# Performance work log

Measured on AMD Instinct MI355X. Metric: run time of the kernel, lower is better.

Reference implementation:

```python
import jax, jax.numpy as jnp
import numpy as np

DIM = 512
K = 64          # num_clusters
GHOST = 1
ALPHA = 100.0
EPS = 1e-12


def _l2norm(v, axis):
    return v / jnp.maximum(jnp.linalg.norm(v, axis=axis, keepdims=True), EPS)


def setup_inputs() -> dict:
    key = jax.random.key(0)
    k_x, k_c = jax.random.split(key)
    x = jax.random.normal(k_x, (64, DIM, 32, 32), dtype=jnp.float32)
    # centroids ~ orthogonal init in torch; random normal rows, unit-ish scale
    centroids = jax.random.normal(k_c, (K + GHOST, DIM), dtype=jnp.float32) / np.sqrt(DIM)
    conv_w = 2.0 * ALPHA * centroids            # [K+g, C] (1x1 conv kernel squeezed)
    conv_b = -ALPHA * jnp.linalg.norm(centroids, axis=1)  # [K+g]
    return {"x": x, "centroids": centroids, "conv_w": conv_w, "conv_b": conv_b}


def reference(x, centroids, conv_w, conv_b):
    N, C, H, W = x.shape
    L = H * W
    # descriptor-wise L2 normalization over channel dim
    xn = _l2norm(x, axis=1)
    xf = xn.reshape(N, C, L)                                   # [N, C, L]
    # 1x1 conv == per-location matmul; softmax over clusters
    logits = jnp.einsum('kc,ncl->nkl', conv_w, xf) + conv_b[None, :, None]
    a = jax.nn.softmax(logits, axis=1)                         # [N, K+g, L]
    # vlad[n,k,c] = sum_l a[n,k,l]*(x[n,c,l]-cent[k,c])
    #            = (a @ x^T) - (sum_l a) * cent   -- avoids NxKxCxL tensor
    weighted = jnp.einsum('nkl,ncl->nkc', a, xf)               # [N, K+g, C]
    a_sum = jnp.sum(a, axis=-1)                                # [N, K+g]
    vlad = weighted - a_sum[:, :, None] * centroids[None]      # [N, K+g, C]
    vlad = vlad[:, :K, :]                                      # drop ghost clusters
    vlad = _l2norm(vlad, axis=2)                               # intra-normalization
    vlad = vlad.reshape(N, K * C)
    vlad = _l2norm(vlad, axis=1)                               # global L2
    return vlad
```

## Files before the change

### kernel.cpp

```cpp
#include <hip/hip_runtime.h>
#include <hip/hip_bf16.h>

#define C_DIM 512
#define L_DIM 1024
#define KK 64
#define KG 65
#define KP 80

using f32x4  = __attribute__((ext_vector_type(4))) float;
using bf16x8 = __attribute__((ext_vector_type(8))) short;

union U4 { uint4 u; bf16x8 b; };

__device__ __forceinline__ unsigned bfh(float x) { return __float_as_uint(x) >> 16; }
__device__ __forceinline__ float bfh_f(float x) { return __uint_as_float(__float_as_uint(x) & 0xFFFF0000u); }

__device__ __forceinline__ unsigned pack2(float a, float b) {
    return __builtin_amdgcn_perm(__float_as_uint(b), __float_as_uint(a), 0x07060302u);
}

__global__ void k_prep(const float* __restrict__ conv_w, const float* __restrict__ conv_b,
                       unsigned short* __restrict__ wpH, unsigned short* __restrict__ wpL,
                       float* __restrict__ wb)
{
    int ch = blockIdx.x;
    int kt = blockIdx.y;
    int t  = threadIdx.x;
    for (int p = 0; p < 2; ++p) {
        int idx = p * 256 + t;
        int lane = idx >> 3, j = idx & 7;
        int k = kt * 16 + (lane & 15);
        int c = ch * 32 + (lane >> 4) * 8 + j;
        float v = (k < KG) ? conv_w[k * C_DIM + c] : 0.f;
        unsigned h = bfh(v);
        float r = v - __uint_as_float(h << 16);
        int pos = ((ch * 5 + kt) << 9) + idx;
        wpH[pos] = (unsigned short)h;
        wpL[pos] = (unsigned short)bfh(r);
    }
    if (ch == 0 && kt == 0 && t < KP) wb[t] = (t < KG) ? conv_b[t] : -1e30f;
}

__global__ __launch_bounds__(256) void k_s1(
    const float* __restrict__ x, const unsigned short* __restrict__ wpH,
    const unsigned short* __restrict__ wpL, const float* __restrict__ wb,
    unsigned short* __restrict__ aPh, unsigned short* __restrict__ aPl,
    float* __restrict__ asum_part)
{
    const int lb = blockIdx.x, n = blockIdx.y;
    const int t = threadIdx.x, lane = t & 63, w = t >> 6;
    const int arow = lane & 15;
    const int agrp = lane >> 4;
    const int lw0 = lb * 128 + w * 32;

    const float* xbase = x + (size_t)n * C_DIM * L_DIM;

    f32x4 acc[5][2];
#pragma unroll
    for (int a = 0; a < 5; ++a)
#pragma unroll
        for (int b = 0; b < 2; ++b) acc[a][b] = (f32x4)0.f;
    float ss0 = 0.f, ss1 = 0.f;

    for (int ch = 0; ch < 16; ++ch) {
        const int c0 = ch * 32;
        float e0[8], e1[8];
#pragma unroll
        for (int j = 0; j < 8; ++j) {
            const float* col = &xbase[(size_t)(c0 + agrp * 8 + j) * L_DIM + lw0 + arow];
            e0[j] = col[0];
            e1[j] = col[16];
        }
#pragma unroll
        for (int j = 0; j < 8; ++j) { ss0 += e0[j] * e0[j]; ss1 += e1[j] * e1[j]; }
        U4 bh[2], bl[2];
        bh[0].u.x = pack2(e0[0], e0[1]); bh[0].u.y = pack2(e0[2], e0[3]);
        bh[0].u.z = pack2(e0[4], e0[5]); bh[0].u.w = pack2(e0[6], e0[7]);
        bh[1].u.x = pack2(e1[0], e1[1]); bh[1].u.y = pack2(e1[2], e1[3]);
        bh[1].u.z = pack2(e1[4], e1[5]); bh[1].u.w = pack2(e1[6], e1[7]);
        float r0, r1, r2, r3;
        r0 = e0[0] - bfh_f(e0[0]); r1 = e0[1] - bfh_f(e0[1]);
        r2 = e0[2] - bfh_f(e0[2]); r3 = e0[3] - bfh_f(e0[3]);
        bl[0].u.x = pack2(r0, r1); bl[0].u.y = pack2(r2, r3);
        r0 = e0[4] - bfh_f(e0[4]); r1 = e0[5] - bfh_f(e0[5]);
        r2 = e0[6] - bfh_f(e0[6]); r3 = e0[7] - bfh_f(e0[7]);
        bl[0].u.z = pack2(r0, r1); bl[0].u.w = pack2(r2, r3);
        r0 = e1[0] - bfh_f(e1[0]); r1 = e1[1] - bfh_f(e1[1]);
        r2 = e1[2] - bfh_f(e1[2]); r3 = e1[3] - bfh_f(e1[3]);
        bl[1].u.x = pack2(r0, r1); bl[1].u.y = pack2(r2, r3);
        r0 = e1[4] - bfh_f(e1[4]); r1 = e1[5] - bfh_f(e1[5]);
        r2 = e1[6] - bfh_f(e1[6]); r3 = e1[7] - bfh_f(e1[7]);
        bl[1].u.z = pack2(r0, r1); bl[1].u.w = pack2(r2, r3);
        U4 ah[5], al[5];
#pragma unroll
        for (int kt = 0; kt < 5; ++kt) {
            int poff = (((ch * 5 + kt) << 6) + lane) << 3;
            ah[kt].u = *reinterpret_cast<const uint4*>(&wpH[poff]);
            al[kt].u = *reinterpret_cast<const uint4*>(&wpL[poff]);
        }
#pragma unroll
        for (int kt = 0; kt < 5; ++kt)
#pragma unroll
            for (int lt = 0; lt < 2; ++lt) {
                acc[kt][lt] = __builtin_amdgcn_mfma_f32_16x16x32_bf16(ah[kt].b, bh[lt].b, acc[kt][lt], 0, 0, 0);
                acc[kt][lt] = __builtin_amdgcn_mfma_f32_16x16x32_bf16(ah[kt].b, bl[lt].b, acc[kt][lt], 0, 0, 0);
                acc[kt][lt] = __builtin_amdgcn_mfma_f32_16x16x32_bf16(al[kt].b, bh[lt].b, acc[kt][lt], 0, 0, 0);
            }
    }

    ss0 += __shfl_xor(ss0, 16, 64); ss0 += __shfl_xor(ss0, 32, 64);
    ss1 += __shfl_xor(ss1, 16, 64); ss1 += __shfl_xor(ss1, 32, 64);
    float invc[2];
    invc[0] = 1.0f / fmaxf(sqrtf(ss0), 1e-12f);
    invc[1] = 1.0f / fmaxf(sqrtf(ss1), 1e-12f);

    float4 wbv[5];
#pragma unroll
    for (int kt = 0; kt < 5; ++kt)
        wbv[kt] = *reinterpret_cast<const float4*>(&wb[kt * 16 + agrp * 4]);

    float aval[5][2][4];
    float rs[2];
#pragma unroll
    for (int lt = 0; lt < 2; ++lt) {
        float m = -1e30f;
#pragma unroll
        for (int kt = 0; kt < 5; ++kt)
#pragma unroll
            for (int r = 0; r < 4; ++r) {
                float lg = acc[kt][lt][r] * invc[lt] + ((const float*)&wbv[kt])[r];
                aval[kt][lt][r] = lg;
                m = fmaxf(m, lg);
            }
        m = fmaxf(m, __shfl_xor(m, 16, 64));
        m = fmaxf(m, __shfl_xor(m, 32, 64));
        float s = 0.f;
#pragma unroll
        for (int kt = 0; kt < 5; ++kt)
#pragma unroll
            for (int r = 0; r < 4; ++r) {
                float e = __expf(aval[kt][lt][r] - m);
                aval[kt][lt][r] = e;
                s += e;
            }
        s += __shfl_xor(s, 16, 64);
        s += __shfl_xor(s, 32, 64);
        rs[lt] = 1.0f / s;
    }

#pragma unroll
    for (int kt = 0; kt < 4; ++kt)
#pragma unroll
        for (int r = 0; r < 4; ++r) {
            int k = kt * 16 + agrp * 4 + r;
            float s01 = 0.f;
#pragma unroll
            for (int lt = 0; lt < 2; ++lt) {
                float a = aval[kt][lt][r] * rs[lt];
                aval[kt][lt][r] = a;
                s01 += a;
            }
#pragma unroll
            for (int off = 8; off; off >>= 1) s01 += __shfl_xor(s01, off, 64);
            if ((lane & 15) == 0)
                asum_part[((n * 8 + lb) * 4 + w) * KK + k] = s01;
#pragma unroll
            for (int lt = 0; lt < 2; ++lt) {
                float ap = aval[kt][lt][r] * invc[lt];
                unsigned h = bfh(ap);
                float res = ap - __uint_as_float(h << 16);
                int idx = (n * KK + k) * L_DIM + lw0 + lt * 16 + arow;
                aPh[idx] = (unsigned short)h;
                aPl[idx] = (unsigned short)bfh(res);
            }
        }
}

#define S2P 72
__global__ __launch_bounds__(256) void k_s2(
    const float* __restrict__ x, const unsigned short* __restrict__ aPh,
    const unsigned short* __restrict__ aPl, float* __restrict__ weighted)
{
    __shared__ unsigned short Ah[64 * S2P], Al[64 * S2P];
    __shared__ unsigned short Bh[64 * S2P], Bl[64 * S2P];

    const int flat = blockIdx.x;
    const int cq = flat >> 6;
    const int n  = ((flat & 7) << 3) | ((flat >> 3) & 7);
    const int t = threadIdx.x, lane = t & 63, w = t >> 6;
    const int arow = lane & 15, agrp = lane >> 4;

    f32x4 acc[4];
#pragma unroll
    for (int a = 0; a < 4; ++a) acc[a] = (f32x4)0.f;

    for (int step = 0; step < 16; ++step) {
        const int l0 = step * 64;
        __syncthreads();
#pragma unroll
        for (int p = 0; p < 2; ++p) {
            int idx = p * 256 + t;
            int k = idx >> 3;
            int lc = (idx & 7) * 8;
            size_t g = (size_t)(n * KK + k) * L_DIM + l0 + lc;
            *reinterpret_cast<uint4*>(&Ah[k * S2P + lc]) = *reinterpret_cast<const uint4*>(&aPh[g]);
            *reinterpret_cast<uint4*>(&Al[k * S2P + lc]) = *reinterpret_cast<const uint4*>(&aPl[g]);
        }
#pragma unroll
        for (int p = 0; p < 4; ++p) {
            int idx = p * 256 + t;
            int c = idx >> 4;
            int lc = (idx & 15) * 4;
            float4 v = *reinterpret_cast<const float4*>(
                &x[((size_t)n * C_DIM + cq * 64 + c) * L_DIM + l0 + lc]);
            uint2 hw, lw;
            hw.x = pack2(v.x, v.y); hw.y = pack2(v.z, v.w);
            float r0 = v.x - bfh_f(v.x), r1 = v.y - bfh_f(v.y);
            float r2 = v.z - bfh_f(v.z), r3 = v.w - bfh_f(v.w);
            lw.x = pack2(r0, r1); lw.y = pack2(r2, r3);
            *reinterpret_cast<uint2*>(&Bh[c * S2P + lc]) = hw;
            *reinterpret_cast<uint2*>(&Bl[c * S2P + lc]) = lw;
        }
        __syncthreads();
#pragma unroll
        for (int ks = 0; ks < 2; ++ks) {
            const int koff = ks * 32 + agrp * 8;
            U4 bh, bl;
            bh.u = *reinterpret_cast<const uint4*>(&Bh[(w * 16 + arow) * S2P + koff]);
            bl.u = *reinterpret_cast<const uint4*>(&Bl[(w * 16 + arow) * S2P + koff]);
#pragma unroll
            for (int kt = 0; kt < 4; ++kt) {
                U4 ah, al;
                ah.u = *reinterpret_cast<const uint4*>(&Ah[(kt * 16 + arow) * S2P + koff]);
                al.u = *reinterpret_cast<const uint4*>(&Al[(kt * 16 + arow) * S2P + koff]);
                acc[kt] = __builtin_amdgcn_mfma_f32_16x16x32_bf16(ah.b, bh.b, acc[kt], 0, 0, 0);
                acc[kt] = __builtin_amdgcn_mfma_f32_16x16x32_bf16(ah.b, bl.b, acc[kt], 0, 0, 0);
                acc[kt] = __builtin_amdgcn_mfma_f32_16x16x32_bf16(al.b, bh.b, acc[kt], 0, 0, 0);
            }
        }
    }
#pragma unroll
    for (int kt = 0; kt < 4; ++kt)
#pragma unroll
        for (int r = 0; r < 4; ++r) {
            int k = kt * 16 + agrp * 4 + r;
            weighted[((size_t)n * KK + k) * C_DIM + cq * 64 + w * 16 + arow] = acc[kt][r];
        }
}

__global__ void k_rownorm(const float* __restrict__ weighted, const float* __restrict__ part,
                          const float* __restrict__ cent, float* __restrict__ a_sum,
                          float* __restrict__ rn)
{
    int nk = blockIdx.x;
    int n = nk >> 6, k = nk & 63;
    int t = threadIdx.x;
    float as = 0.f;
#pragma unroll
    for (int p = 0; p < 32; ++p) as += part[(n * 32 + p) * KK + k];
    if (t == 0) a_sum[nk] = as;
    float s = 0.f;
    for (int c = t; c < C_DIM; c += 256) {
        float v = weighted[(size_t)nk * C_DIM + c] - as * cent[k * C_DIM + c];
        s += v * v;
    }
#pragma unroll
    for (int off = 32; off; off >>= 1) s += __shfl_down(s, off, 64);
    __shared__ float red[4];
    if ((t & 63) == 0) red[t >> 6] = s;
    __syncthreads();
    if (t == 0) rn[nk] = red[0] + red[1] + red[2] + red[3];
}

__global__ void k_scale(const float* __restrict__ rn, float* __restrict__ scale)
{
    int n = blockIdx.x;
    int k = threadIdx.x;
    float s = rn[n * 64 + k];
    float nrm = sqrtf(s);
    float den = fmaxf(nrm, 1e-12f);
    float tk = nrm / den;
    float tot = tk * tk;
#pragma unroll
    for (int off = 32; off; off >>= 1) tot += __shfl_down(tot, off, 64);
    tot = __shfl(tot, 0, 64);
    float g = fmaxf(sqrtf(tot), 1e-12f);
    scale[n * 64 + k] = 1.0f / (den * g);
}

__global__ void k_out(const float* __restrict__ weighted, const float* __restrict__ a_sum,
                      const float* __restrict__ cent, const float* __restrict__ scale,
                      float* __restrict__ out)
{
    int nk = blockIdx.x;
    int k = nk & 63;
    int t = threadIdx.x;
    float as = a_sum[nk];
    float sc = scale[nk];
    for (int c = t; c < C_DIM; c += 256) {
        float v = weighted[(size_t)nk * C_DIM + c] - as * cent[k * C_DIM + c];
        out[(size_t)nk * C_DIM + c] = v * sc;
    }
}

extern "C" void kernel_launch(void* const* d_in, const int* in_sizes, int n_in,
                              void* d_out, int out_size, void* d_ws, size_t ws_size,
                              hipStream_t stream)
{
    const float* x    = (const float*)d_in[0];
    const float* cent = (const float*)d_in[1];
    const float* cw   = (const float*)d_in[2];
    const float* cb   = (const float*)d_in[3];
    float* out = (float*)d_out;
    char* ws = (char*)d_ws;

    unsigned short* wpH = (unsigned short*)(ws + 0);
    unsigned short* wpL = (unsigned short*)(ws + 131072);
    float*          wb  = (float*)(ws + 262144);
    unsigned short* aPh = (unsigned short*)(ws + 524288);
    unsigned short* aPl = (unsigned short*)(ws + 8912896);
    float* asum_part    = (float*)(ws + 17301504);
    float* a_sum        = (float*)(ws + 17825792);
    float* weighted     = (float*)(ws + 18874368);
    float* rn           = (float*)(ws + 35651584);
    float* scale        = (float*)(ws + 35667968);

    k_prep<<<dim3(16, 5), 256, 0, stream>>>(cw, cb, wpH, wpL, wb);
    k_s1<<<dim3(8, 64), 256, 0, stream>>>(x, wpH, wpL, wb, aPh, aPl, asum_part);
    k_s2<<<512, 256, 0, stream>>>(x, aPh, aPl, weighted);
    k_rownorm<<<4096, 256, 0, stream>>>(weighted, asum_part, cent, a_sum, rn);
    k_scale<<<64, 64, 0, stream>>>(rn, scale);
    k_out<<<4096, 256, 0, stream>>>(weighted, a_sum, cent, scale, out);
}
```

Baseline: 78.45 us.

## Split first-stage logits GEMM over channel halves with partial-sum reduction kernel

The logits stage is split into two kernels. The first runs twice as many blocks, each covering half the channel range, and writes partial MFMA accumulators and squared-norm sums to workspace. The second kernel adds the two partials and then does the softmax and packing. This is meant to fill the GPU better than 512 blocks did, at the cost of an extra launch and an extra round trip of partials through global memory.

```diff
diff --git a/kernel.cpp b/kernel.cpp
--- a/kernel.cpp
+++ b/kernel.cpp
@@ -18,6 +18,8 @@
 __device__ __forceinline__ unsigned pack2(float a, float b) {
     return __builtin_amdgcn_perm(__float_as_uint(b), __float_as_uint(a), 0x07060302u);
 }
+
+#define PB 2688
 
 __global__ void k_prep(const float* __restrict__ conv_w, const float* __restrict__ conv_b,
                        unsigned short* __restrict__ wpH, unsigned short* __restrict__ wpL,
@@ -41,13 +43,12 @@
     if (ch == 0 && kt == 0 && t < KP) wb[t] = (t < KG) ? conv_b[t] : -1e30f;
 }
 
-__global__ __launch_bounds__(256) void k_s1(
+__global__ __launch_bounds__(256) void k_s1a(
     const float* __restrict__ x, const unsigned short* __restrict__ wpH,
-    const unsigned short* __restrict__ wpL, const float* __restrict__ wb,
-    unsigned short* __restrict__ aPh, unsigned short* __restrict__ aPl,
-    float* __restrict__ asum_part)
-{
-    const int lb = blockIdx.x, n = blockIdx.y;
+    const unsigned short* __restrict__ wpL, float* __restrict__ pacc)
+{
+    const int bx = blockIdx.x, n = blockIdx.y;
+    const int lb = bx >> 1, chalf = bx & 1;
     const int t = threadIdx.x, lane = t & 63, w = t >> 6;
     const int arow = lane & 15;
     const int agrp = lane >> 4;
@@ -62,7 +63,8 @@
         for (int b = 0; b < 2; ++b) acc[a][b] = (f32x4)0.f;
     float ss0 = 0.f, ss1 = 0.f;
 
-    for (int ch = 0; ch < 16; ++ch) {
+    for (int ch8 = 0; ch8 < 8; ++ch8) {
+        const int ch = chalf * 8 + ch8;
         const int c0 = ch * 32;
         float e0[8], e1[8];
 #pragma unroll
@@ -108,6 +110,48 @@
             }
     }
 
+    float* p = pacc + ((size_t)(n * 16 + bx) * 4 + w) * PB;
+#pragma unroll
+    for (int kt = 0; kt < 5; ++kt)
+#pragma unroll
+        for (int lt = 0; lt < 2; ++lt)
+            *reinterpret_cast<float4*>(&p[(kt * 2 + lt) * 256 + lane * 4]) =
+                make_float4(acc[kt][lt][0], acc[kt][lt][1], acc[kt][lt][2], acc[kt][lt][3]);
+    *reinterpret_cast<float2*>(&p[2560 + lane * 2]) = make_float2(ss0, ss1);
+}
+
+__global__ __launch_bounds__(256) void k_s1b(
+    const float* __restrict__ pacc, const float* __restrict__ wb,
+    unsigned short* __restrict__ aPh, unsigned short* __restrict__ aPl,
+    float* __restrict__ asum_part)
+{
+    const int lb = blockIdx.x, n = blockIdx.y;
+    const int t = threadIdx.x, lane = t & 63, w = t >> 6;
+    const int arow = lane & 15;
+    const int agrp = lane >> 4;
+    const int lw0 = lb * 128 + w * 32;
+
+    f32x4 acc[5][2];
+    float ss0 = 0.f, ss1 = 0.f;
+#pragma unroll
+    for (int a = 0; a < 5; ++a)
+#pragma unroll
+        for (int b = 0; b < 2; ++b) acc[a][b] = (f32x4)0.f;
+#pragma unroll
+    for (int chalf = 0; chalf < 2; ++chalf) {
+        const float* p = pacc + ((size_t)(n * 16 + lb * 2 + chalf) * 4 + w) * PB;
+#pragma unroll
+        for (int kt = 0; kt < 5; ++kt)
+#pragma unroll
+            for (int lt = 0; lt < 2; ++lt) {
+                float4 v = *reinterpret_cast<const float4*>(&p[(kt * 2 + lt) * 256 + lane * 4]);
+                acc[kt][lt][0] += v.x; acc[kt][lt][1] += v.y;
+                acc[kt][lt][2] += v.z; acc[kt][lt][3] += v.w;
+            }
+        float2 sv = *reinterpret_cast<const float2*>(&p[2560 + lane * 2]);
+        ss0 += sv.x; ss1 += sv.y;
+    }
+
     ss0 += __shfl_xor(ss0, 16, 64); ss0 += __shfl_xor(ss0, 32, 64);
     ss1 += __shfl_xor(ss1, 16, 64); ss1 += __shfl_xor(ss1, 32, 64);
     float invc[2];
@@ -324,9 +368,11 @@
     float* weighted     = (float*)(ws + 18874368);
     float* rn           = (float*)(ws + 35651584);
     float* scale        = (float*)(ws + 35667968);
+    float* pacc         = (float*)(ws + 37748736);
 
     k_prep<<<dim3(16, 5), 256, 0, stream>>>(cw, cb, wpH, wpL, wb);
-    k_s1<<<dim3(8, 64), 256, 0, stream>>>(x, wpH, wpL, wb, aPh, aPl, asum_part);
+    k_s1a<<<dim3(16, 64), 256, 0, stream>>>(x, wpH, wpL, pacc);
+    k_s1b<<<dim3(8, 64), 256, 0, stream>>>(pacc, wb, aPh, aPl, asum_part);
     k_s2<<<512, 256, 0, stream>>>(x, aPh, aPl, weighted);
     k_rownorm<<<4096, 256, 0, stream>>>(weighted, asum_part, cent, a_sum, rn);
     k_scale<<<64, 64, 0, stream>>>(rn, scale);
```

New measurement: 96.69 us. 1.23x slower.
